# Performance work log

Hardware: AMD Instinct MI355X
Metric: run time of the kernel (lower is better)

Reference implementation:

```python
import jax, jax.numpy as jnp
import numpy as np

B, S, D, H, W = 8, 2048, 128, 8, 64
INT_HEADS = 8          # hardcoded in SpatioTemporalLayer1
EPS_COS = 1e-8
EPS_LN = 1e-5


def _mha(q_in, k_in, v_in, in_w, in_b, out_w, out_b, nh, mask=None):
    # q_in/k_in/v_in: (batch, len, d); torch nn.MultiheadAttention math (eval, no dropout)
    b, lq, d = q_in.shape
    hd = d // nh
    q = (q_in @ in_w[:d].T + in_b[:d]).reshape(b, lq, nh, hd)
    k = (k_in @ in_w[d:2 * d].T + in_b[d:2 * d]).reshape(b, k_in.shape[1], nh, hd)
    v = (v_in @ in_w[2 * d:].T + in_b[2 * d:]).reshape(b, v_in.shape[1], nh, hd)
    scores = jnp.einsum('bihd,bjhd->bhij', q, k) / jnp.sqrt(jnp.asarray(hd, q_in.dtype))
    if mask is not None:
        scores = scores + mask
    attn = jax.nn.softmax(scores, axis=-1)
    out = jnp.einsum('bhij,bjhd->bihd', attn, v).reshape(b, lq, d)
    return out @ out_w.T + out_b


def _layernorm(x, g, b):
    mu = x.mean(-1, keepdims=True)
    var = ((x - mu) ** 2).mean(-1, keepdims=True)
    return (x - mu) * jax.lax.rsqrt(var + EPS_LN) * g + b


def _cos_normalize(e):
    n = jnp.maximum(jnp.linalg.norm(e, axis=-1, keepdims=True), EPS_COS)
    return e / n


def _forward(x, spatial_info, temporal_info,
             lw_in_w, lw_in_b, lw_out_w, lw_out_b,
             spat_w, spat_b, temp_w, temp_b,
             int_in_w, int_in_b, int_out_w, int_out_b,
             ffn_w1, ffn_b1, ffn_w2, ffn_b2,
             ln1_g, ln1_b, ln2_g, ln2_b):
    b, s, d = x.shape
    # --- local window attention (S % W == 0 here, so no padding path) ---
    nw = s // W
    xw = x.reshape(b * nw, W, d)
    causal = jnp.triu(jnp.full((W, W), -jnp.inf, x.dtype), k=1)
    attn = _mha(xw, xw, xw, lw_in_w, lw_in_b, lw_out_w, lw_out_b, H, causal).reshape(b, s, d)
    x = _layernorm(attn + x, ln1_g, ln1_b)
    # --- FFN (torch nn.GELU default = exact erf) ---
    h = jax.nn.gelu(x @ ffn_w1.T + ffn_b1, approximate=False)
    x = _layernorm(h @ ffn_w2.T + ffn_b2 + x, ln2_g, ln2_b)
    # --- spatio-temporal interaction ---
    se = spatial_info @ spat_w.T + spat_b
    te = temporal_info @ temp_w.T + temp_b
    sn = _cos_normalize(se)
    tn = _cos_normalize(te)
    ss = jnp.einsum('bid,bjd->bij', sn, sn)   # (B,S,S) spatial cosine sim
    ts = jnp.einsum('bid,bjd->bij', tn, tn)   # (B,S,S) temporal cosine sim
    # interaction MHA is batch_first=False: it treats (B,S,D) as (len=B, batch=S, d).
    # Equivalent batch-first call on swapped axes (faithful to the torch source).
    inter = jnp.swapaxes(
        _mha(jnp.swapaxes(se, 0, 1), jnp.swapaxes(te, 0, 1), jnp.swapaxes(te, 0, 1),
             int_in_w, int_in_b, int_out_w, int_out_b, INT_HEADS), 0, 1)
    # similarity[b,i,j,d] = ss[b,i,j]*ts[b,i,j]*inter[b,i,d]; mean over j factorizes:
    sim = (ss * ts).mean(axis=2)              # (B,S)
    return x + sim[..., None] * inter


def setup_inputs() -> dict:
    key = jax.random.key(0)
    ks = jax.random.split(key, 24)
    sc = 0.02
    inp = {
        'x': jax.random.normal(ks[0], (B, S, D), jnp.float32),
        'spatial_info': jax.random.normal(ks[1], (B, S, D), jnp.float32),
        'temporal_info': jax.random.normal(ks[2], (B, S, D), jnp.float32),
        'lw_in_w': jax.random.normal(ks[3], (3 * D, D), jnp.float32) * sc,
        'lw_in_b': jnp.zeros((3 * D,), jnp.float32),
        'lw_out_w': jax.random.normal(ks[4], (D, D), jnp.float32) * sc,
        'lw_out_b': jnp.zeros((D,), jnp.float32),
        'spat_w': jax.random.normal(ks[5], (D, D), jnp.float32) * sc,
        'spat_b': jnp.zeros((D,), jnp.float32),
        'temp_w': jax.random.normal(ks[6], (D, D), jnp.float32) * sc,
        'temp_b': jnp.zeros((D,), jnp.float32),
        'int_in_w': jax.random.normal(ks[7], (3 * D, D), jnp.float32) * sc,
        'int_in_b': jnp.zeros((3 * D,), jnp.float32),
        'int_out_w': jax.random.normal(ks[8], (D, D), jnp.float32) * sc,
        'int_out_b': jnp.zeros((D,), jnp.float32),
        'ffn_w1': jax.random.normal(ks[9], (4 * D, D), jnp.float32) * sc,
        'ffn_b1': jnp.zeros((4 * D,), jnp.float32),
        'ffn_w2': jax.random.normal(ks[10], (D, 4 * D), jnp.float32) * sc,
        'ffn_b2': jnp.zeros((D,), jnp.float32),
        'ln1_g': jnp.ones((D,), jnp.float32),
        'ln1_b': jnp.zeros((D,), jnp.float32),
        'ln2_g': jnp.ones((D,), jnp.float32),
        'ln2_b': jnp.zeros((D,), jnp.float32),
    }
    return inp


def reference(x, spatial_info, temporal_info,
              lw_in_w, lw_in_b, lw_out_w, lw_out_b,
              spat_w, spat_b, temp_w, temp_b,
              int_in_w, int_in_b, int_out_w, int_out_b,
              ffn_w1, ffn_b1, ffn_w2, ffn_b2,
              ln1_g, ln1_b, ln2_g, ln2_b):
    return _forward(x, spatial_info, temporal_info,
                    lw_in_w, lw_in_b, lw_out_w, lw_out_b,
                    spat_w, spat_b, temp_w, temp_b,
                    int_in_w, int_in_b, int_out_w, int_out_b,
                    ffn_w1, ffn_b1, ffn_w2, ffn_b2,
                    ln1_g, ln1_b, ln2_g, ln2_b)
```

## Files before the change

### kernel.cpp

```cpp
#include <hip/hip_runtime.h>
#include <math.h>

#define BB 8
#define SS 2048
#define NTOK (BB * SS)
#define ATB_SPLIT 16

using bf16x8 = __attribute__((ext_vector_type(8))) short;
using f32x4  = __attribute__((ext_vector_type(4))) float;

__device__ __forceinline__ float gelu_tanh(float x) {
    float y = 0.7978845608f * (x + 0.044715f * x * x * x);
    float e = __expf(2.0f * y);
    float t = 1.0f - 2.0f / (e + 1.0f);
    return 0.5f * x * (1.0f + t);
}
__device__ __forceinline__ unsigned short f2b(float f) {
    unsigned int u = __float_as_uint(f);
    u += 0x7FFFu + ((u >> 16) & 1u);
    return (unsigned short)(u >> 16);
}
__device__ __forceinline__ float b2f(unsigned short u) {
    return __uint_as_float((unsigned int)u << 16);
}
__device__ __forceinline__ bf16x8 ldg_f32_b8(const float* p) {
    float4 f0 = *(const float4*)p, f1 = *(const float4*)(p + 4);
    union { ushort4 u[2]; bf16x8 v; } r;
    r.u[0] = (ushort4){f2b(f0.x), f2b(f0.y), f2b(f0.z), f2b(f0.w)};
    r.u[1] = (ushort4){f2b(f1.x), f2b(f1.y), f2b(f1.z), f2b(f1.w)};
    return r.v;
}

__global__ __launch_bounds__(256) void phaseA(
    const float* __restrict__ x,
    const float* __restrict__ lw_in_w, const float* __restrict__ b_in,
    const float* __restrict__ lw_out_w, const float* __restrict__ b_out,
    const float* __restrict__ lng, const float* __restrict__ lnb,
    float* __restrict__ x1, unsigned short* __restrict__ x1b,
    const float* __restrict__ ffn_w1, const float* __restrict__ ffn_w2,
    unsigned short* __restrict__ Wb)
{
    __shared__ unsigned short Qs[64 * 136];
    __shared__ unsigned short Ks[64 * 136];
    __shared__ unsigned short Vt[128 * 72];
    __shared__ unsigned short Pb[4][32 * 72];
    __shared__ float red[2][64][2];
    const int tid = threadIdx.x;

    if (blockIdx.x >= 256) {
        int i = (blockIdx.x - 256) * 256 + tid;
        float v = (i < 65536) ? ffn_w1[i] : ffn_w2[i - 65536];
        Wb[i] = f2b(v);
        return;
    }

    const int m0 = blockIdx.x * 64;
    const int wv = tid >> 6, lane = tid & 63, ln = lane & 15, q = lane >> 4;
    const int wm = (wv >> 1) * 32, wn = (wv & 1) * 64;

    bf16x8 afr[4][2];
    #pragma unroll
    for (int kf = 0; kf < 4; ++kf)
        #pragma unroll
        for (int fm = 0; fm < 2; ++fm)
            afr[kf][fm] = ldg_f32_b8(x + (size_t)(m0 + wm + fm * 16 + ln) * 128 + kf * 32 + q * 8);

    #pragma unroll
    for (int p = 0; p < 3; ++p) {
        f32x4 acc[2][4] = {};
        #pragma unroll
        for (int kf = 0; kf < 4; ++kf) {
            bf16x8 b[4];
            #pragma unroll
            for (int fn = 0; fn < 4; ++fn)
                b[fn] = ldg_f32_b8(lw_in_w + (size_t)(p * 128 + wn + fn * 16 + ln) * 128 + kf * 32 + q * 8);
            #pragma unroll
            for (int fm = 0; fm < 2; ++fm)
                #pragma unroll
                for (int fn = 0; fn < 4; ++fn)
                    acc[fm][fn] = __builtin_amdgcn_mfma_f32_16x16x32_bf16(afr[kf][fm], b[fn], acc[fm][fn], 0, 0, 0);
        }
        #pragma unroll
        for (int fm = 0; fm < 2; ++fm)
            #pragma unroll
            for (int r = 0; r < 4; ++r) {
                int rl = wm + fm * 16 + q * 4 + r;
                #pragma unroll
                for (int fn = 0; fn < 4; ++fn) {
                    int col = wn + fn * 16 + ln;
                    unsigned short v = f2b(acc[fm][fn][r] + b_in[p * 128 + col]);
                    if (p == 0)      Qs[rl * 136 + col] = v;
                    else if (p == 1) Ks[rl * 136 + col] = v;
                    else             Vt[col * 72 + rl] = v;
                }
            }
    }
    __syncthreads();

    {
        const int mh = wv >> 1, hq = wv & 1;
        unsigned short* P = &Pb[wv][0];
        #pragma unroll
        for (int hh = 0; hh < 4; ++hh) {
            const int h = hq * 4 + hh;
            f32x4 sacc[2][4] = {};
            bf16x8 az[2] = {}, bz[4] = {};
            if (q < 2) {
                #pragma unroll
                for (int fm = 0; fm < 2; ++fm)
                    az[fm] = *(const bf16x8*)&Qs[(mh * 32 + fm * 16 + ln) * 136 + h * 16 + q * 8];
                #pragma unroll
                for (int fn = 0; fn < 4; ++fn)
                    bz[fn] = *(const bf16x8*)&Ks[(fn * 16 + ln) * 136 + h * 16 + q * 8];
            }
            #pragma unroll
            for (int fm = 0; fm < 2; ++fm)
                #pragma unroll
                for (int fn = 0; fn < 4; ++fn)
                    sacc[fm][fn] = __builtin_amdgcn_mfma_f32_16x16x32_bf16(az[fm], bz[fn], sacc[fm][fn], 0, 0, 0);
            float invr[2][4];
            #pragma unroll
            for (int fm = 0; fm < 2; ++fm)
                #pragma unroll
                for (int r = 0; r < 4; ++r) {
                    int gi = mh * 32 + fm * 16 + q * 4 + r;
                    float mx = -1e30f;
                    #pragma unroll
                    for (int fn = 0; fn < 4; ++fn) {
                        int j = fn * 16 + ln;
                        float s = sacc[fm][fn][r] * 0.25f;
                        if (j > gi) s = -1e30f;
                        sacc[fm][fn][r] = s;
                        mx = fmaxf(mx, s);
                    }
                    #pragma unroll
                    for (int off = 1; off < 16; off <<= 1)
                        mx = fmaxf(mx, __shfl_xor(mx, off, 64));
                    float sum = 0.0f;
                    #pragma unroll
                    for (int fn = 0; fn < 4; ++fn) {
                        float p_ = __expf(sacc[fm][fn][r] - mx);
                        sacc[fm][fn][r] = p_;
                        sum += p_;
                    }
                    #pragma unroll
                    for (int off = 1; off < 16; off <<= 1)
                        sum += __shfl_xor(sum, off, 64);
                    invr[fm][r] = 1.0f / sum;
                    #pragma unroll
                    for (int fn = 0; fn < 4; ++fn)
                        P[(fm * 16 + q * 4 + r) * 72 + fn * 16 + ln] = f2b(sacc[fm][fn][r]);
                }
            f32x4 oacc[2] = {};
            #pragma unroll
            for (int kf2 = 0; kf2 < 2; ++kf2) {
                bf16x8 pa[2], vb;
                #pragma unroll
                for (int fm = 0; fm < 2; ++fm)
                    pa[fm] = *(const bf16x8*)&P[(fm * 16 + ln) * 72 + kf2 * 32 + q * 8];
                vb = *(const bf16x8*)&Vt[(h * 16 + ln) * 72 + kf2 * 32 + q * 8];
                #pragma unroll
                for (int fm = 0; fm < 2; ++fm)
                    oacc[fm] = __builtin_amdgcn_mfma_f32_16x16x32_bf16(pa[fm], vb, oacc[fm], 0, 0, 0);
            }
            #pragma unroll
            for (int fm = 0; fm < 2; ++fm)
                #pragma unroll
                for (int r = 0; r < 4; ++r)
                    Qs[(mh * 32 + fm * 16 + q * 4 + r) * 136 + h * 16 + ln] =
                        f2b(oacc[fm][r] * invr[fm][r]);
        }
    }
    __syncthreads();

    f32x4 acc[2][4] = {};
    #pragma unroll
    for (int kf = 0; kf < 4; ++kf) {
        bf16x8 a[2], b[4];
        #pragma unroll
        for (int fm = 0; fm < 2; ++fm)
            a[fm] = *(const bf16x8*)&Qs[(wm + fm * 16 + ln) * 136 + kf * 32 + q * 8];
        #pragma unroll
        for (int fn = 0; fn < 4; ++fn)
            b[fn] = ldg_f32_b8(lw_out_w + (size_t)(wn + fn * 16 + ln) * 128 + kf * 32 + q * 8);
        #pragma unroll
        for (int fm = 0; fm < 2; ++fm)
            #pragma unroll
            for (int fn = 0; fn < 4; ++fn)
                acc[fm][fn] = __builtin_amdgcn_mfma_f32_16x16x32_bf16(a[fm], b[fn], acc[fm][fn], 0, 0, 0);
    }
    #pragma unroll
    for (int fm = 0; fm < 2; ++fm)
        #pragma unroll
        for (int r = 0; r < 4; ++r) {
            int rl = wm + fm * 16 + q * 4 + r;
            int row = m0 + rl;
            float s1 = 0.0f, s2 = 0.0f;
            #pragma unroll
            for (int fn = 0; fn < 4; ++fn) {
                int col = wn + fn * 16 + ln;
                float vv = acc[fm][fn][r] + b_out[col] + x[(size_t)row * 128 + col];
                acc[fm][fn][r] = vv;
                s1 += vv; s2 += vv * vv;
            }
            #pragma unroll
            for (int off = 1; off < 16; off <<= 1) {
                s1 += __shfl_xor(s1, off, 64);
                s2 += __shfl_xor(s2, off, 64);
            }
            if (ln == 0) { red[0][rl][wv & 1] = s1; red[1][rl][wv & 1] = s2; }
        }
    __syncthreads();
    #pragma unroll
    for (int fm = 0; fm < 2; ++fm)
        #pragma unroll
        for (int r = 0; r < 4; ++r) {
            int rl = wm + fm * 16 + q * 4 + r;
            int row = m0 + rl;
            float mu = (red[0][rl][0] + red[0][rl][1]) * (1.0f / 128.0f);
            float var = (red[1][rl][0] + red[1][rl][1]) * (1.0f / 128.0f) - mu * mu;
            float rs = rsqrtf(var + 1e-5f);
            #pragma unroll
            for (int fn = 0; fn < 4; ++fn) {
                int col = wn + fn * 16 + ln;
                float o = (acc[fm][fn][r] - mu) * rs * lng[col] + lnb[col];
                x1[(size_t)row * 128 + col] = o;
                x1b[(size_t)row * 128 + col] = f2b(o);
            }
        }
}

__global__ __launch_bounds__(256) void ffn_fused(
    const unsigned short* __restrict__ x1b, const float* __restrict__ x1,
    const unsigned short* __restrict__ w1, const unsigned short* __restrict__ w2,
    const float* __restrict__ b1, const float* __restrict__ b2,
    const float* __restrict__ lng, const float* __restrict__ lnb,
    float* __restrict__ x2)
{
    __shared__ unsigned short Xs[64 * 136];
    __shared__ unsigned short Hs[2][64 * 72];
    __shared__ float red[2][64][2];
    const int tid = threadIdx.x, t0 = blockIdx.x * 64;
    const int wv = tid >> 6, lane = tid & 63, ln = lane & 15, q = lane >> 4;
    const int wm = (wv >> 1) * 32;
    const int wn1 = (wv & 1) * 32, wn2 = (wv & 1) * 64;

    const uint4* X4 = (const uint4*)(x1b + (size_t)t0 * 128);
    #pragma unroll
    for (int t = 0; t < 4; ++t) {
        int idx = tid + t * 256;
        int r = idx >> 4, c = idx & 15;
        *(uint4*)&Xs[r * 136 + c * 8] = X4[r * 16 + c];
    }
    __syncthreads();

    bf16x8 xfr[4][2];
    #pragma unroll
    for (int kf = 0; kf < 4; ++kf)
        #pragma unroll
        for (int fm = 0; fm < 2; ++fm)
            xfr[kf][fm] = *(const bf16x8*)&Xs[(wm + fm * 16 + ln) * 136 + kf * 32 + q * 8];

    f32x4 acc2[2][4] = {};
    for (int ch = 0; ch < 8; ++ch) {
        const int hc0 = ch * 64;
        unsigned short* Hb = &Hs[ch & 1][0];
        f32x4 acc1[2][2] = {};
        #pragma unroll
        for (int kf = 0; kf < 4; ++kf) {
            bf16x8 b[2];
            #pragma unroll
            for (int fn = 0; fn < 2; ++fn)
                b[fn] = *(const bf16x8*)&w1[(size_t)(hc0 + wn1 + fn * 16 + ln) * 128 + kf * 32 + q * 8];
            #pragma unroll
            for (int fm = 0; fm < 2; ++fm)
                #pragma unroll
                for (int fn = 0; fn < 2; ++fn)
                    acc1[fm][fn] = __builtin_amdgcn_mfma_f32_16x16x32_bf16(xfr[kf][fm], b[fn], acc1[fm][fn], 0, 0, 0);
        }
        #pragma unroll
        for (int fm = 0; fm < 2; ++fm)
            #pragma unroll
            for (int fn = 0; fn < 2; ++fn)
                #pragma unroll
                for (int r = 0; r < 4; ++r) {
                    int rl = wm + fm * 16 + q * 4 + r;
                    int col = wn1 + fn * 16 + ln;
                    Hb[rl * 72 + col] = f2b(gelu_tanh(acc1[fm][fn][r] + b1[hc0 + col]));
                }
        __syncthreads();
        #pragma unroll
        for (int kf2 = 0; kf2 < 2; ++kf2) {
            bf16x8 a[2], b[4];
            #pragma unroll
            for (int fm = 0; fm < 2; ++fm)
                a[fm] = *(const bf16x8*)&Hb[(wm + fm * 16 + ln) * 72 + kf2 * 32 + q * 8];
            #pragma unroll
            for (int fn = 0; fn < 4; ++fn)
                b[fn] = *(const bf16x8*)&w2[(size_t)(wn2 + fn * 16 + ln) * 512 + hc0 + kf2 * 32 + q * 8];
            #pragma unroll
            for (int fm = 0; fm < 2; ++fm)
                #pragma unroll
                for (int fn = 0; fn < 4; ++fn)
                    acc2[fm][fn] = __builtin_amdgcn_mfma_f32_16x16x32_bf16(a[fm], b[fn], acc2[fm][fn], 0, 0, 0);
        }
    }
    #pragma unroll
    for (int fm = 0; fm < 2; ++fm)
        #pragma unroll
        for (int r = 0; r < 4; ++r) {
            int rl = wm + fm * 16 + q * 4 + r;
            int row = t0 + rl;
            float s1 = 0.0f, s2 = 0.0f;
            #pragma unroll
            for (int fn = 0; fn < 4; ++fn) {
                int col = wn2 + fn * 16 + ln;
                float vv = acc2[fm][fn][r] + b2[col] + x1[(size_t)row * 128 + col];
                acc2[fm][fn][r] = vv;
                s1 += vv; s2 += vv * vv;
            }
            #pragma unroll
            for (int off = 1; off < 16; off <<= 1) {
                s1 += __shfl_xor(s1, off, 64);
                s2 += __shfl_xor(s2, off, 64);
            }
            if (ln == 0) { red[0][rl][wv & 1] = s1; red[1][rl][wv & 1] = s2; }
        }
    __syncthreads();
    #pragma unroll
    for (int fm = 0; fm < 2; ++fm)
        #pragma unroll
        for (int r = 0; r < 4; ++r) {
            int rl = wm + fm * 16 + q * 4 + r;
            int row = t0 + rl;
            float mu = (red[0][rl][0] + red[0][rl][1]) * (1.0f / 128.0f);
            float var = (red[1][rl][0] + red[1][rl][1]) * (1.0f / 128.0f) - mu * mu;
            float rs = rsqrtf(var + 1e-5f);
            #pragma unroll
            for (int fn = 0; fn < 4; ++fn) {
                int col = wn2 + fn * 16 + ln;
                x2[(size_t)row * 128 + col] = (acc2[fm][fn][r] - mu) * rs * lng[col] + lnb[col];
            }
        }
}

__global__ __launch_bounds__(256) void stproj_kernel(
    const float* __restrict__ sp, const float* __restrict__ tp,
    const float* __restrict__ Wsp, const float* __restrict__ Wtp,
    const float* __restrict__ bsp, const float* __restrict__ btp,
    unsigned short* __restrict__ snb, unsigned short* __restrict__ tnb,
    unsigned short* __restrict__ seb, unsigned short* __restrict__ teb)
{
    __shared__ float red[64][2];
    const int tid = threadIdx.x, m0 = blockIdx.x * 64, y = blockIdx.y;
    const float* Af = y ? tp : sp;
    const float* Wf = y ? Wtp : Wsp;
    const float* bias = y ? btp : bsp;
    unsigned short* nb = y ? tnb : snb;
    unsigned short* raw = y ? teb : seb;
    const int wv = tid >> 6, lane = tid & 63, ln = lane & 15, q = lane >> 4;
    const int wm = (wv >> 1) * 32, wn = (wv & 1) * 64;

    f32x4 acc[2][4] = {};
    #pragma unroll
    for (int kf = 0; kf < 4; ++kf) {
        bf16x8 a[2], b[4];
        #pragma unroll
        for (int fm = 0; fm < 2; ++fm)
            a[fm] = ldg_f32_b8(Af + (size_t)(m0 + wm + fm * 16 + ln) * 128 + kf * 32 + q * 8);
        #pragma unroll
        for (int fn = 0; fn < 4; ++fn)
            b[fn] = ldg_f32_b8(Wf + (size_t)(wn + fn * 16 + ln) * 128 + kf * 32 + q * 8);
        #pragma unroll
        for (int fm = 0; fm < 2; ++fm)
            #pragma unroll
            for (int fn = 0; fn < 4; ++fn)
                acc[fm][fn] = __builtin_amdgcn_mfma_f32_16x16x32_bf16(a[fm], b[fn], acc[fm][fn], 0, 0, 0);
    }
    #pragma unroll
    for (int fm = 0; fm < 2; ++fm)
        #pragma unroll
        for (int r = 0; r < 4; ++r) {
            int rl = wm + fm * 16 + q * 4 + r;
            float s2 = 0.0f;
            #pragma unroll
            for (int fn = 0; fn < 4; ++fn) {
                int col = wn + fn * 16 + ln;
                float vv = acc[fm][fn][r] + bias[col];
                acc[fm][fn][r] = vv;
                s2 += vv * vv;
            }
            #pragma unroll
            for (int off = 1; off < 16; off <<= 1) s2 += __shfl_xor(s2, off, 64);
            if (ln == 0) red[rl][wv & 1] = s2;
        }
    __syncthreads();
    #pragma unroll
    for (int fm = 0; fm < 2; ++fm)
        #pragma unroll
        for (int r = 0; r < 4; ++r) {
            int rl = wm + fm * 16 + q * 4 + r;
            int row = m0 + rl;
            float inv = 1.0f / fmaxf(sqrtf(red[rl][0] + red[rl][1]), 1e-8f);
            #pragma unroll
            for (int fn = 0; fn < 4; ++fn) {
                int col = wn + fn * 16 + ln;
                float vv = acc[fm][fn][r];
                nb[(size_t)row * 128 + col] = f2b(vv * inv);
                raw[(size_t)row * 128 + col] = f2b(vv);
            }
        }
}

__global__ __launch_bounds__(256) void atb_split_kernel(
    const unsigned short* __restrict__ snb, const unsigned short* __restrict__ tnb,
    float* __restrict__ part)
{
    const int b = blockIdx.z / ATB_SPLIT;
    const int chunk = blockIdx.z % ATB_SPLIT;
    const int d0 = blockIdx.x * 64, e0 = blockIdx.y * 64;
    __shared__ float Ss[32][68];
    __shared__ float Ts[32][68];
    const int tid = threadIdx.x;
    const int tx = tid % 16, ty = tid / 16;
    const int jbase = chunk * (SS / ATB_SPLIT);
    float acc[4][4] = {};
    for (int j0 = jbase; j0 < jbase + SS / ATB_SPLIT; j0 += 32) {
        {
            int r = tid >> 3, c8 = (tid & 7) * 8;
            uint4 sv = *(const uint4*)&snb[(size_t)(b * SS + j0 + r) * 128 + d0 + c8];
            uint4 tv = *(const uint4*)&tnb[(size_t)(b * SS + j0 + r) * 128 + e0 + c8];
            const unsigned short* sp = (const unsigned short*)&sv;
            const unsigned short* tp = (const unsigned short*)&tv;
            #pragma unroll
            for (int c = 0; c < 8; ++c) {
                Ss[r][c8 + c] = b2f(sp[c]);
                Ts[r][c8 + c] = b2f(tp[c]);
            }
        }
        __syncthreads();
        #pragma unroll
        for (int kk = 0; kk < 32; ++kk) {
            float4 af = *(const float4*)&Ss[kk][ty * 4];
            float4 wf = *(const float4*)&Ts[kk][tx * 4];
            float a[4] = {af.x, af.y, af.z, af.w};
            float w[4] = {wf.x, wf.y, wf.z, wf.w};
            #pragma unroll
            for (int i = 0; i < 4; ++i)
                #pragma unroll
                for (int j = 0; j < 4; ++j)
                    acc[i][j] = fmaf(a[i], w[j], acc[i][j]);
        }
        __syncthreads();
    }
    float* pp = part + (size_t)(b * ATB_SPLIT + chunk) * 16384;
    #pragma unroll
    for (int i = 0; i < 4; ++i) {
        float4 ov = {acc[i][0], acc[i][1], acc[i][2], acc[i][3]};
        *(float4*)&pp[(size_t)(d0 + ty * 4 + i) * 128 + e0 + tx * 4] = ov;
    }
}

__global__ __launch_bounds__(256) void atb_reduce_kernel(
    const float* __restrict__ part, unsigned short* __restrict__ Mtb)
{
    int i = blockIdx.x * 256 + threadIdx.x;
    int b = i >> 14, rem = i & 16383;
    int e = rem >> 7, d = rem & 127;
    const float* pp = part + (size_t)b * ATB_SPLIT * 16384 + (size_t)d * 128 + e;
    float s = 0.0f;
    #pragma unroll
    for (int c = 0; c < ATB_SPLIT; ++c) s += pp[(size_t)c * 16384];
    Mtb[i] = f2b(s);
}

__global__ __launch_bounds__(256) void simgemm_kernel(
    const unsigned short* __restrict__ snb, const unsigned short* __restrict__ tnb,
    const unsigned short* __restrict__ Mtb, float* __restrict__ sim)
{
    __shared__ float red[64][2];
    const int tid = threadIdx.x, m0 = blockIdx.x * 64, b = m0 >> 11;
    const int wv = tid >> 6, lane = tid & 63, ln = lane & 15, q = lane >> 4;
    const int wm = (wv >> 1) * 32, wn = (wv & 1) * 64;

    f32x4 acc[2][4] = {};
    #pragma unroll
    for (int kf = 0; kf < 4; ++kf) {
        bf16x8 a[2], bb[4];
        #pragma unroll
        for (int fm = 0; fm < 2; ++fm)
            a[fm] = *(const bf16x8*)&snb[(size_t)(m0 + wm + fm * 16 + ln) * 128 + kf * 32 + q * 8];
        #pragma unroll
        for (int fn = 0; fn < 4; ++fn)
            bb[fn] = *(const bf16x8*)&Mtb[(size_t)b * 16384 + (size_t)(wn + fn * 16 + ln) * 128 + kf * 32 + q * 8];
        #pragma unroll
        for (int fm = 0; fm < 2; ++fm)
            #pragma unroll
            for (int fn = 0; fn < 4; ++fn)
                acc[fm][fn] = __builtin_amdgcn_mfma_f32_16x16x32_bf16(a[fm], bb[fn], acc[fm][fn], 0, 0, 0);
    }
    #pragma unroll
    for (int fm = 0; fm < 2; ++fm)
        #pragma unroll
        for (int r = 0; r < 4; ++r) {
            int rl = wm + fm * 16 + q * 4 + r;
            int row = m0 + rl;
            float s = 0.0f;
            #pragma unroll
            for (int fn = 0; fn < 4; ++fn) {
                int col = wn + fn * 16 + ln;
                s += acc[fm][fn][r] * b2f(tnb[(size_t)row * 128 + col]);
            }
            #pragma unroll
            for (int off = 1; off < 16; off <<= 1) s += __shfl_xor(s, off, 64);
            if (ln == 0) red[rl][wv & 1] = s;
        }
    __syncthreads();
    if (tid < 64) sim[m0 + tid] = (red[tid][0] + red[tid][1]) * (1.0f / (float)SS);
}

__global__ __launch_bounds__(256) void inter_block(
    const unsigned short* __restrict__ seb, const unsigned short* __restrict__ teb,
    const float* __restrict__ Wint,
    const float* __restrict__ b_int,
    const float* __restrict__ Wio,
    const float* __restrict__ b_io,
    const float* __restrict__ sim, const float* __restrict__ x2,
    float* __restrict__ out)
{
    __shared__ unsigned short Qs[64 * 136];
    __shared__ unsigned short KVs[64 * 256];
    const int tid = threadIdx.x, s0 = blockIdx.x * 8;
    const int wv = tid >> 6, lane = tid & 63, ln = lane & 15, q = lane >> 4;
    const int wm = (wv >> 1) * 32, wn = (wv & 1) * 64;

    bf16x8 afr[4][2];
    #pragma unroll
    for (int kf = 0; kf < 4; ++kf)
        #pragma unroll
        for (int fm = 0; fm < 2; ++fm) {
            int rl = wm + fm * 16 + ln;
            size_t g = (size_t)(rl >> 3) * 2048 + s0 + (rl & 7);
            afr[kf][fm] = *(const bf16x8*)&seb[g * 128 + kf * 32 + q * 8];
        }

    #pragma unroll
    for (int p = 0; p < 3; ++p) {
        if (p == 1) {
            #pragma unroll
            for (int kf = 0; kf < 4; ++kf)
                #pragma unroll
                for (int fm = 0; fm < 2; ++fm) {
                    int rl = wm + fm * 16 + ln;
                    size_t g = (size_t)(rl >> 3) * 2048 + s0 + (rl & 7);
                    afr[kf][fm] = *(const bf16x8*)&teb[g * 128 + kf * 32 + q * 8];
                }
        }
        f32x4 acc[2][4] = {};
        #pragma unroll
        for (int kf = 0; kf < 4; ++kf) {
            bf16x8 b[4];
            #pragma unroll
            for (int fn = 0; fn < 4; ++fn)
                b[fn] = ldg_f32_b8(Wint + (size_t)(p * 128 + wn + fn * 16 + ln) * 128 + kf * 32 + q * 8);
            #pragma unroll
            for (int fm = 0; fm < 2; ++fm)
                #pragma unroll
                for (int fn = 0; fn < 4; ++fn)
                    acc[fm][fn] = __builtin_amdgcn_mfma_f32_16x16x32_bf16(afr[kf][fm], b[fn], acc[fm][fn], 0, 0, 0);
        }
        #pragma unroll
        for (int fm = 0; fm < 2; ++fm)
            #pragma unroll
            for (int r = 0; r < 4; ++r) {
                int rl = wm + fm * 16 + q * 4 + r;
                #pragma unroll
                for (int fn = 0; fn < 4; ++fn) {
                    int col = wn + fn * 16 + ln;
                    unsigned short v = f2b(acc[fm][fn][r] + b_int[p * 128 + col]);
                    if (p == 0) Qs[rl * 136 + col] = v;
                    else        KVs[rl * 256 + (p - 1) * 128 + col] = v;
                }
            }
        __syncthreads();
    }

    #pragma unroll
    for (int tt = 0; tt < 2; ++tt) {
        int task = tid + tt * 256;
        int ss = task >> 6, h = (task >> 3) & 7, i = task & 7;
        int rq = i * 8 + ss;
        float qr[16];
        {
            uint4 q0 = *(const uint4*)&Qs[rq * 136 + h * 16];
            uint4 q1 = *(const uint4*)&Qs[rq * 136 + h * 16 + 8];
            const unsigned short* p0 = (const unsigned short*)&q0;
            const unsigned short* p1 = (const unsigned short*)&q1;
            #pragma unroll
            for (int c = 0; c < 8; ++c) { qr[c] = b2f(p0[c]); qr[8 + c] = b2f(p1[c]); }
        }
        float sc[8];
        #pragma unroll
        for (int j = 0; j < 8; ++j) {
            uint4 k0 = *(const uint4*)&KVs[(j * 8 + ss) * 256 + h * 16];
            uint4 k1 = *(const uint4*)&KVs[(j * 8 + ss) * 256 + h * 16 + 8];
            const unsigned short* kp0 = (const unsigned short*)&k0;
            const unsigned short* kp1 = (const unsigned short*)&k1;
            float s = 0.0f;
            #pragma unroll
            for (int c = 0; c < 8; ++c) {
                s = fmaf(qr[c], b2f(kp0[c]), s);
                s = fmaf(qr[8 + c], b2f(kp1[c]), s);
            }
            sc[j] = s * 0.25f;
        }
        float mx = -1e30f;
        #pragma unroll
        for (int j = 0; j < 8; ++j) mx = fmaxf(mx, sc[j]);
        float pe[8], se = 0.0f;
        #pragma unroll
        for (int j = 0; j < 8; ++j) { pe[j] = __expf(sc[j] - mx); se += pe[j]; }
        float inv = 1.0f / se;
        float o[16] = {};
        #pragma unroll
        for (int j = 0; j < 8; ++j) {
            uint4 v0 = *(const uint4*)&KVs[(j * 8 + ss) * 256 + 128 + h * 16];
            uint4 v1 = *(const uint4*)&KVs[(j * 8 + ss) * 256 + 128 + h * 16 + 8];
            const unsigned short* vp0 = (const unsigned short*)&v0;
            const unsigned short* vp1 = (const unsigned short*)&v1;
            #pragma unroll
            for (int c = 0; c < 8; ++c) {
                o[c]     += pe[j] * b2f(vp0[c]);
                o[8 + c] += pe[j] * b2f(vp1[c]);
            }
        }
        ushort4 w0 = (ushort4){f2b(o[0]*inv),  f2b(o[1]*inv),  f2b(o[2]*inv),  f2b(o[3]*inv)};
        ushort4 w1 = (ushort4){f2b(o[4]*inv),  f2b(o[5]*inv),  f2b(o[6]*inv),  f2b(o[7]*inv)};
        ushort4 w2 = (ushort4){f2b(o[8]*inv),  f2b(o[9]*inv),  f2b(o[10]*inv), f2b(o[11]*inv)};
        ushort4 w3 = (ushort4){f2b(o[12]*inv), f2b(o[13]*inv), f2b(o[14]*inv), f2b(o[15]*inv)};
        *(ushort4*)&Qs[rq * 136 + h * 16]      = w0;
        *(ushort4*)&Qs[rq * 136 + h * 16 + 4]  = w1;
        *(ushort4*)&Qs[rq * 136 + h * 16 + 8]  = w2;
        *(ushort4*)&Qs[rq * 136 + h * 16 + 12] = w3;
    }
    __syncthreads();

    f32x4 acc[2][4] = {};
    #pragma unroll
    for (int kf = 0; kf < 4; ++kf) {
        bf16x8 a[2], b[4];
        #pragma unroll
        for (int fm = 0; fm < 2; ++fm)
            a[fm] = *(const bf16x8*)&Qs[(wm + fm * 16 + ln) * 136 + kf * 32 + q * 8];
        #pragma unroll
        for (int fn = 0; fn < 4; ++fn)
            b[fn] = ldg_f32_b8(Wio + (size_t)(wn + fn * 16 + ln) * 128 + kf * 32 + q * 8);
        #pragma unroll
        for (int fm = 0; fm < 2; ++fm)
            #pragma unroll
            for (int fn = 0; fn < 4; ++fn)
                acc[fm][fn] = __builtin_amdgcn_mfma_f32_16x16x32_bf16(a[fm], b[fn], acc[fm][fn], 0, 0, 0);
    }
    #pragma unroll
    for (int fm = 0; fm < 2; ++fm)
        #pragma unroll
        for (int r = 0; r < 4; ++r) {
            int rl = wm + fm * 16 + q * 4 + r;
            size_t g = (size_t)(rl >> 3) * 2048 + s0 + (rl & 7);
            float sc = sim[g];
            #pragma unroll
            for (int fn = 0; fn < 4; ++fn) {
                int col = wn + fn * 16 + ln;
                out[g * 128 + col] = (acc[fm][fn][r] + b_io[col]) * sc + x2[g * 128 + col];
            }
        }
}

extern "C" void kernel_launch(void* const* d_in, const int* in_sizes, int n_in,
                              void* d_out, int out_size, void* d_ws, size_t ws_size,
                              hipStream_t stream)
{
    const float* x        = (const float*)d_in[0];
    const float* spatial  = (const float*)d_in[1];
    const float* temporal = (const float*)d_in[2];
    const float* lw_in_w  = (const float*)d_in[3];
    const float* lw_in_b  = (const float*)d_in[4];
    const float* lw_out_w = (const float*)d_in[5];
    const float* lw_out_b = (const float*)d_in[6];
    const float* spat_w   = (const float*)d_in[7];
    const float* spat_b   = (const float*)d_in[8];
    const float* temp_w   = (const float*)d_in[9];
    const float* temp_b   = (const float*)d_in[10];
    const float* int_in_w = (const float*)d_in[11];
    const float* int_in_b = (const float*)d_in[12];
    const float* int_out_w= (const float*)d_in[13];
    const float* int_out_b= (const float*)d_in[14];
    const float* ffn_w1   = (const float*)d_in[15];
    const float* ffn_b1   = (const float*)d_in[16];
    const float* ffn_w2   = (const float*)d_in[17];
    const float* ffn_b2   = (const float*)d_in[18];
    const float* ln1_g    = (const float*)d_in[19];
    const float* ln1_b    = (const float*)d_in[20];
    const float* ln2_g    = (const float*)d_in[21];
    const float* ln2_b    = (const float*)d_in[22];
    float* out = (float*)d_out;

    char* base = (char*)d_ws;
    float*          x1   = (float*)(base + 0);
    unsigned short* x1b  = (unsigned short*)(base + 8388608);
    float*          x2   = (float*)(base + 12582912);
    unsigned short* snb  = (unsigned short*)(base + 20971520);
    unsigned short* tnb  = (unsigned short*)(base + 25165824);
    unsigned short* seb  = (unsigned short*)(base + 29360128);
    unsigned short* teb  = (unsigned short*)(base + 33554432);
    unsigned short* Mtb  = (unsigned short*)(base + 37748736);
    float*          simb = (float*)(base + 38010880);
    unsigned short* Wb   = (unsigned short*)(base + 38076416);
    float*          part = x1;

    phaseA<<<768, 256, 0, stream>>>(
        x, lw_in_w, lw_in_b, lw_out_w, lw_out_b, ln1_g, ln1_b, x1, x1b,
        ffn_w1, ffn_w2, Wb);
    ffn_fused<<<256, 256, 0, stream>>>(
        x1b, x1, Wb, Wb + 65536, ffn_b1, ffn_b2, ln2_g, ln2_b, x2);
    stproj_kernel<<<dim3(256, 2), 256, 0, stream>>>(
        spatial, temporal, spat_w, temp_w, spat_b, temp_b,
        snb, tnb, seb, teb);
    atb_split_kernel<<<dim3(2, 2, 8 * ATB_SPLIT), 256, 0, stream>>>(snb, tnb, part);
    atb_reduce_kernel<<<512, 256, 0, stream>>>(part, Mtb);
    simgemm_kernel<<<256, 256, 0, stream>>>(snb, tnb, Mtb, simb);
    inter_block<<<2048 / 8, 256, 0, stream>>>(
        seb, teb, int_in_w, int_in_b, int_out_w, int_out_b, simb, x2, out);
}
```

Before: 249.3 us.

## Merge independent kernels into two heterogeneous launches to cut launch count

Folds the spatial/temporal projection and normalization into the first kernel as extra blocks alongside windowed attention and weight conversion. Folds the split A^T B partial reduction into the FFN kernel as extra blocks, using a shared memory pool. The partials buffer moves to its own workspace region because it can no longer alias x1 while the FFN reads it. This removes two launches and lets independent work overlap across CUs, at the cost of higher shared-memory footprint for the smaller block types and a larger workspace.

```diff
diff --git a/kernel.cpp b/kernel.cpp
--- a/kernel.cpp
+++ b/kernel.cpp
@@ -31,14 +31,19 @@
     return r.v;
 }
 
-__global__ __launch_bounds__(256) void phaseA(
+__global__ __launch_bounds__(256) void phase1(
     const float* __restrict__ x,
     const float* __restrict__ lw_in_w, const float* __restrict__ b_in,
     const float* __restrict__ lw_out_w, const float* __restrict__ b_out,
     const float* __restrict__ lng, const float* __restrict__ lnb,
     float* __restrict__ x1, unsigned short* __restrict__ x1b,
     const float* __restrict__ ffn_w1, const float* __restrict__ ffn_w2,
-    unsigned short* __restrict__ Wb)
+    unsigned short* __restrict__ Wb,
+    const float* __restrict__ spatial, const float* __restrict__ temporal,
+    const float* __restrict__ spat_w, const float* __restrict__ temp_w,
+    const float* __restrict__ bsp, const float* __restrict__ btp,
+    unsigned short* __restrict__ snb, unsigned short* __restrict__ tnb,
+    unsigned short* __restrict__ seb, unsigned short* __restrict__ teb)
 {
     __shared__ unsigned short Qs[64 * 136];
     __shared__ unsigned short Ks[64 * 136];
@@ -46,6 +51,70 @@
     __shared__ unsigned short Pb[4][32 * 72];
     __shared__ float red[2][64][2];
     const int tid = threadIdx.x;
+    const int wv = tid >> 6, lane = tid & 63, ln = lane & 15, q = lane >> 4;
+
+    if (blockIdx.x >= 768) {
+        const int idx2 = blockIdx.x - 768;
+        const int y = idx2 >> 8;
+        const int m0 = (idx2 & 255) * 64;
+        const float* Af = y ? temporal : spatial;
+        const float* Wf = y ? temp_w : spat_w;
+        const float* bias = y ? btp : bsp;
+        unsigned short* nb = y ? tnb : snb;
+        unsigned short* raw = y ? teb : seb;
+        const int wm = (wv >> 1) * 32, wn = (wv & 1) * 64;
+
+        f32x4 acc[2][4] = {};
+        #pragma unroll
+        for (int kf = 0; kf < 4; ++kf) {
+            bf16x8 a[2], b[4];
+            #pragma unroll
+            for (int fm = 0; fm < 2; ++fm)
+                a[fm] = ldg_f32_b8(Af + (size_t)(m0 + wm + fm * 16 + ln) * 128 + kf * 32 + q * 8);
+            #pragma unroll
+            for (int fn = 0; fn < 4; ++fn)
+                b[fn] = ldg_f32_b8(Wf + (size_t)(wn + fn * 16 + ln) * 128 + kf * 32 + q * 8);
+            #pragma unroll
+            for (int fm = 0; fm < 2; ++fm)
+                #pragma unroll
+                for (int fn = 0; fn < 4; ++fn)
+                    acc[fm][fn] = __builtin_amdgcn_mfma_f32_16x16x32_bf16(a[fm], b[fn], acc[fm][fn], 0, 0, 0);
+        }
+        #pragma unroll
+        for (int fm = 0; fm < 2; ++fm)
+            #pragma unroll
+            for (int r = 0; r < 4; ++r) {
+                int rl = wm + fm * 16 + q * 4 + r;
+                float s2 = 0.0f;
+                #pragma unroll
+                for (int fn = 0; fn < 4; ++fn) {
+                    int col = wn + fn * 16 + ln;
+                    float vv = acc[fm][fn][r] + bias[col];
+                    acc[fm][fn][r] = vv;
+                    s2 += vv * vv;
+                }
+                #pragma unroll
+                for (int off = 1; off < 16; off <<= 1) s2 += __shfl_xor(s2, off, 64);
+                if (ln == 0) red[0][rl][wv & 1] = s2;
+            }
+        __syncthreads();
+        #pragma unroll
+        for (int fm = 0; fm < 2; ++fm)
+            #pragma unroll
+            for (int r = 0; r < 4; ++r) {
+                int rl = wm + fm * 16 + q * 4 + r;
+                int row = m0 + rl;
+                float inv = 1.0f / fmaxf(sqrtf(red[0][rl][0] + red[0][rl][1]), 1e-8f);
+                #pragma unroll
+                for (int fn = 0; fn < 4; ++fn) {
+                    int col = wn + fn * 16 + ln;
+                    float vv = acc[fm][fn][r];
+                    nb[(size_t)row * 128 + col] = f2b(vv * inv);
+                    raw[(size_t)row * 128 + col] = f2b(vv);
+                }
+            }
+        return;
+    }
 
     if (blockIdx.x >= 256) {
         int i = (blockIdx.x - 256) * 256 + tid;
@@ -55,7 +124,6 @@
     }
 
     const int m0 = blockIdx.x * 64;
-    const int wv = tid >> 6, lane = tid & 63, ln = lane & 15, q = lane >> 4;
     const int wm = (wv >> 1) * 32, wn = (wv & 1) * 64;
 
     bf16x8 afr[4][2];
@@ -230,234 +298,174 @@
         }
 }
 
-__global__ __launch_bounds__(256) void ffn_fused(
+__global__ __launch_bounds__(256) void phase2(
     const unsigned short* __restrict__ x1b, const float* __restrict__ x1,
-    const unsigned short* __restrict__ w1, const unsigned short* __restrict__ w2,
+    const unsigned short* __restrict__ Wb,
     const float* __restrict__ b1, const float* __restrict__ b2,
     const float* __restrict__ lng, const float* __restrict__ lnb,
-    float* __restrict__ x2)
-{
-    __shared__ unsigned short Xs[64 * 136];
-    __shared__ unsigned short Hs[2][64 * 72];
-    __shared__ float red[2][64][2];
-    const int tid = threadIdx.x, t0 = blockIdx.x * 64;
-    const int wv = tid >> 6, lane = tid & 63, ln = lane & 15, q = lane >> 4;
-    const int wm = (wv >> 1) * 32;
-    const int wn1 = (wv & 1) * 32, wn2 = (wv & 1) * 64;
-
-    const uint4* X4 = (const uint4*)(x1b + (size_t)t0 * 128);
-    #pragma unroll
-    for (int t = 0; t < 4; ++t) {
-        int idx = tid + t * 256;
-        int r = idx >> 4, c = idx & 15;
-        *(uint4*)&Xs[r * 136 + c * 8] = X4[r * 16 + c];
-    }
-    __syncthreads();
-
-    bf16x8 xfr[4][2];
-    #pragma unroll
-    for (int kf = 0; kf < 4; ++kf)
-        #pragma unroll
-        for (int fm = 0; fm < 2; ++fm)
-            xfr[kf][fm] = *(const bf16x8*)&Xs[(wm + fm * 16 + ln) * 136 + kf * 32 + q * 8];
-
-    f32x4 acc2[2][4] = {};
-    for (int ch = 0; ch < 8; ++ch) {
-        const int hc0 = ch * 64;
-        unsigned short* Hb = &Hs[ch & 1][0];
-        f32x4 acc1[2][2] = {};
-        #pragma unroll
-        for (int kf = 0; kf < 4; ++kf) {
-            bf16x8 b[2];
-            #pragma unroll
-            for (int fn = 0; fn < 2; ++fn)
-                b[fn] = *(const bf16x8*)&w1[(size_t)(hc0 + wn1 + fn * 16 + ln) * 128 + kf * 32 + q * 8];
-            #pragma unroll
-            for (int fm = 0; fm < 2; ++fm)
-                #pragma unroll
-                for (int fn = 0; fn < 2; ++fn)
-                    acc1[fm][fn] = __builtin_amdgcn_mfma_f32_16x16x32_bf16(xfr[kf][fm], b[fn], acc1[fm][fn], 0, 0, 0);
-        }
-        #pragma unroll
-        for (int fm = 0; fm < 2; ++fm)
-            #pragma unroll
-            for (int fn = 0; fn < 2; ++fn)
-                #pragma unroll
-                for (int r = 0; r < 4; ++r) {
-                    int rl = wm + fm * 16 + q * 4 + r;
-                    int col = wn1 + fn * 16 + ln;
-                    Hb[rl * 72 + col] = f2b(gelu_tanh(acc1[fm][fn][r] + b1[hc0 + col]));
-                }
-        __syncthreads();
-        #pragma unroll
-        for (int kf2 = 0; kf2 < 2; ++kf2) {
-            bf16x8 a[2], b[4];
-            #pragma unroll
-            for (int fm = 0; fm < 2; ++fm)
-                a[fm] = *(const bf16x8*)&Hb[(wm + fm * 16 + ln) * 72 + kf2 * 32 + q * 8];
-            #pragma unroll
-            for (int fn = 0; fn < 4; ++fn)
-                b[fn] = *(const bf16x8*)&w2[(size_t)(wn2 + fn * 16 + ln) * 512 + hc0 + kf2 * 32 + q * 8];
-            #pragma unroll
-            for (int fm = 0; fm < 2; ++fm)
-                #pragma unroll
-                for (int fn = 0; fn < 4; ++fn)
-                    acc2[fm][fn] = __builtin_amdgcn_mfma_f32_16x16x32_bf16(a[fm], b[fn], acc2[fm][fn], 0, 0, 0);
-        }
-    }
-    #pragma unroll
-    for (int fm = 0; fm < 2; ++fm)
-        #pragma unroll
-        for (int r = 0; r < 4; ++r) {
-            int rl = wm + fm * 16 + q * 4 + r;
-            int row = t0 + rl;
-            float s1 = 0.0f, s2 = 0.0f;
-            #pragma unroll
-            for (int fn = 0; fn < 4; ++fn) {
-                int col = wn2 + fn * 16 + ln;
-                float vv = acc2[fm][fn][r] + b2[col] + x1[(size_t)row * 128 + col];
-                acc2[fm][fn][r] = vv;
-                s1 += vv; s2 += vv * vv;
-            }
-            #pragma unroll
-            for (int off = 1; off < 16; off <<= 1) {
-                s1 += __shfl_xor(s1, off, 64);
-                s2 += __shfl_xor(s2, off, 64);
-            }
-            if (ln == 0) { red[0][rl][wv & 1] = s1; red[1][rl][wv & 1] = s2; }
-        }
-    __syncthreads();
-    #pragma unroll
-    for (int fm = 0; fm < 2; ++fm)
-        #pragma unroll
-        for (int r = 0; r < 4; ++r) {
-            int rl = wm + fm * 16 + q * 4 + r;
-            int row = t0 + rl;
-            float mu = (red[0][rl][0] + red[0][rl][1]) * (1.0f / 128.0f);
-            float var = (red[1][rl][0] + red[1][rl][1]) * (1.0f / 128.0f) - mu * mu;
-            float rs = rsqrtf(var + 1e-5f);
-            #pragma unroll
-            for (int fn = 0; fn < 4; ++fn) {
-                int col = wn2 + fn * 16 + ln;
-                x2[(size_t)row * 128 + col] = (acc2[fm][fn][r] - mu) * rs * lng[col] + lnb[col];
-            }
-        }
-}
-
-__global__ __launch_bounds__(256) void stproj_kernel(
-    const float* __restrict__ sp, const float* __restrict__ tp,
-    const float* __restrict__ Wsp, const float* __restrict__ Wtp,
-    const float* __restrict__ bsp, const float* __restrict__ btp,
-    unsigned short* __restrict__ snb, unsigned short* __restrict__ tnb,
-    unsigned short* __restrict__ seb, unsigned short* __restrict__ teb)
-{
-    __shared__ float red[64][2];
-    const int tid = threadIdx.x, m0 = blockIdx.x * 64, y = blockIdx.y;
-    const float* Af = y ? tp : sp;
-    const float* Wf = y ? Wtp : Wsp;
-    const float* bias = y ? btp : bsp;
-    unsigned short* nb = y ? tnb : snb;
-    unsigned short* raw = y ? teb : seb;
-    const int wv = tid >> 6, lane = tid & 63, ln = lane & 15, q = lane >> 4;
-    const int wm = (wv >> 1) * 32, wn = (wv & 1) * 64;
-
-    f32x4 acc[2][4] = {};
-    #pragma unroll
-    for (int kf = 0; kf < 4; ++kf) {
-        bf16x8 a[2], b[4];
-        #pragma unroll
-        for (int fm = 0; fm < 2; ++fm)
-            a[fm] = ldg_f32_b8(Af + (size_t)(m0 + wm + fm * 16 + ln) * 128 + kf * 32 + q * 8);
-        #pragma unroll
-        for (int fn = 0; fn < 4; ++fn)
-            b[fn] = ldg_f32_b8(Wf + (size_t)(wn + fn * 16 + ln) * 128 + kf * 32 + q * 8);
-        #pragma unroll
-        for (int fm = 0; fm < 2; ++fm)
-            #pragma unroll
-            for (int fn = 0; fn < 4; ++fn)
-                acc[fm][fn] = __builtin_amdgcn_mfma_f32_16x16x32_bf16(a[fm], b[fn], acc[fm][fn], 0, 0, 0);
-    }
-    #pragma unroll
-    for (int fm = 0; fm < 2; ++fm)
-        #pragma unroll
-        for (int r = 0; r < 4; ++r) {
-            int rl = wm + fm * 16 + q * 4 + r;
-            float s2 = 0.0f;
-            #pragma unroll
-            for (int fn = 0; fn < 4; ++fn) {
-                int col = wn + fn * 16 + ln;
-                float vv = acc[fm][fn][r] + bias[col];
-                acc[fm][fn][r] = vv;
-                s2 += vv * vv;
-            }
-            #pragma unroll
-            for (int off = 1; off < 16; off <<= 1) s2 += __shfl_xor(s2, off, 64);
-            if (ln == 0) red[rl][wv & 1] = s2;
-        }
-    __syncthreads();
-    #pragma unroll
-    for (int fm = 0; fm < 2; ++fm)
-        #pragma unroll
-        for (int r = 0; r < 4; ++r) {
-            int rl = wm + fm * 16 + q * 4 + r;
-            int row = m0 + rl;
-            float inv = 1.0f / fmaxf(sqrtf(red[rl][0] + red[rl][1]), 1e-8f);
-            #pragma unroll
-            for (int fn = 0; fn < 4; ++fn) {
-                int col = wn + fn * 16 + ln;
-                float vv = acc[fm][fn][r];
-                nb[(size_t)row * 128 + col] = f2b(vv * inv);
-                raw[(size_t)row * 128 + col] = f2b(vv);
-            }
-        }
-}
-
-__global__ __launch_bounds__(256) void atb_split_kernel(
+    float* __restrict__ x2,
     const unsigned short* __restrict__ snb, const unsigned short* __restrict__ tnb,
     float* __restrict__ part)
 {
-    const int b = blockIdx.z / ATB_SPLIT;
-    const int chunk = blockIdx.z % ATB_SPLIT;
-    const int d0 = blockIdx.x * 64, e0 = blockIdx.y * 64;
-    __shared__ float Ss[32][68];
-    __shared__ float Ts[32][68];
+    __shared__ __align__(16) char pool[36864];
+    __shared__ float red[2][64][2];
     const int tid = threadIdx.x;
-    const int tx = tid % 16, ty = tid / 16;
-    const int jbase = chunk * (SS / ATB_SPLIT);
-    float acc[4][4] = {};
-    for (int j0 = jbase; j0 < jbase + SS / ATB_SPLIT; j0 += 32) {
-        {
-            int r = tid >> 3, c8 = (tid & 7) * 8;
-            uint4 sv = *(const uint4*)&snb[(size_t)(b * SS + j0 + r) * 128 + d0 + c8];
-            uint4 tv = *(const uint4*)&tnb[(size_t)(b * SS + j0 + r) * 128 + e0 + c8];
-            const unsigned short* sp = (const unsigned short*)&sv;
-            const unsigned short* tp = (const unsigned short*)&tv;
-            #pragma unroll
-            for (int c = 0; c < 8; ++c) {
-                Ss[r][c8 + c] = b2f(sp[c]);
-                Ts[r][c8 + c] = b2f(tp[c]);
-            }
+    const int wv = tid >> 6, lane = tid & 63, ln = lane & 15, q = lane >> 4;
+
+    if (blockIdx.x < 256) {
+        unsigned short* Xs = (unsigned short*)pool;
+        unsigned short* Hs0 = (unsigned short*)(pool + 17408);
+        unsigned short* Hs1 = (unsigned short*)(pool + 26624);
+        const int t0 = blockIdx.x * 64;
+        const int wm = (wv >> 1) * 32;
+        const int wn1 = (wv & 1) * 32, wn2 = (wv & 1) * 64;
+        const unsigned short* w1 = Wb;
+        const unsigned short* w2 = Wb + 65536;
+
+        const uint4* X4 = (const uint4*)(x1b + (size_t)t0 * 128);
+        #pragma unroll
+        for (int t = 0; t < 4; ++t) {
+            int idx = tid + t * 256;
+            int r = idx >> 4, c = idx & 15;
+            *(uint4*)&Xs[r * 136 + c * 8] = X4[r * 16 + c];
         }
         __syncthreads();
-        #pragma unroll
-        for (int kk = 0; kk < 32; ++kk) {
-            float4 af = *(const float4*)&Ss[kk][ty * 4];
-            float4 wf = *(const float4*)&Ts[kk][tx * 4];
-            float a[4] = {af.x, af.y, af.z, af.w};
-            float w[4] = {wf.x, wf.y, wf.z, wf.w};
-            #pragma unroll
-            for (int i = 0; i < 4; ++i)
-                #pragma unroll
-                for (int j = 0; j < 4; ++j)
-                    acc[i][j] = fmaf(a[i], w[j], acc[i][j]);
-        }
+
+        bf16x8 xfr[4][2];
+        #pragma unroll
+        for (int kf = 0; kf < 4; ++kf)
+            #pragma unroll
+            for (int fm = 0; fm < 2; ++fm)
+                xfr[kf][fm] = *(const bf16x8*)&Xs[(wm + fm * 16 + ln) * 136 + kf * 32 + q * 8];
+
+        f32x4 acc2[2][4] = {};
+        for (int ch = 0; ch < 8; ++ch) {
+            const int hc0 = ch * 64;
+            unsigned short* Hb = (ch & 1) ? Hs1 : Hs0;
+            f32x4 acc1[2][2] = {};
+            #pragma unroll
+            for (int kf = 0; kf < 4; ++kf) {
+                bf16x8 b[2];
+                #pragma unroll
+                for (int fn = 0; fn < 2; ++fn)
+                    b[fn] = *(const bf16x8*)&w1[(size_t)(hc0 + wn1 + fn * 16 + ln) * 128 + kf * 32 + q * 8];
+                #pragma unroll
+                for (int fm = 0; fm < 2; ++fm)
+                    #pragma unroll
+                    for (int fn = 0; fn < 2; ++fn)
+                        acc1[fm][fn] = __builtin_amdgcn_mfma_f32_16x16x32_bf16(xfr[kf][fm], b[fn], acc1[fm][fn], 0, 0, 0);
+            }
+            #pragma unroll
+            for (int fm = 0; fm < 2; ++fm)
+                #pragma unroll
+                for (int fn = 0; fn < 2; ++fn)
+                    #pragma unroll
+                    for (int r = 0; r < 4; ++r) {
+                        int rl = wm + fm * 16 + q * 4 + r;
+                        int col = wn1 + fn * 16 + ln;
+                        Hb[rl * 72 + col] = f2b(gelu_tanh(acc1[fm][fn][r] + b1[hc0 + col]));
+                    }
+            __syncthreads();
+            #pragma unroll
+            for (int kf2 = 0; kf2 < 2; ++kf2) {
+                bf16x8 a[2], b[4];
+                #pragma unroll
+                for (int fm = 0; fm < 2; ++fm)
+                    a[fm] = *(const bf16x8*)&Hb[(wm + fm * 16 + ln) * 72 + kf2 * 32 + q * 8];
+                #pragma unroll
+                for (int fn = 0; fn < 4; ++fn)
+                    b[fn] = *(const bf16x8*)&w2[(size_t)(wn2 + fn * 16 + ln) * 512 + hc0 + kf2 * 32 + q * 8];
+                #pragma unroll
+                for (int fm = 0; fm < 2; ++fm)
+                    #pragma unroll
+                    for (int fn = 0; fn < 4; ++fn)
+                        acc2[fm][fn] = __builtin_amdgcn_mfma_f32_16x16x32_bf16(a[fm], b[fn], acc2[fm][fn], 0, 0, 0);
+            }
+        }
+        #pragma unroll
+        for (int fm = 0; fm < 2; ++fm)
+            #pragma unroll
+            for (int r = 0; r < 4; ++r) {
+                int rl = wm + fm * 16 + q * 4 + r;
+                int row = t0 + rl;
+                float s1 = 0.0f, s2 = 0.0f;
+                #pragma unroll
+                for (int fn = 0; fn < 4; ++fn) {
+                    int col = wn2 + fn * 16 + ln;
+                    float vv = acc2[fm][fn][r] + b2[col] + x1[(size_t)row * 128 + col];
+                    acc2[fm][fn][r] = vv;
+                    s1 += vv; s2 += vv * vv;
+                }
+                #pragma unroll
+                for (int off = 1; off < 16; off <<= 1) {
+                    s1 += __shfl_xor(s1, off, 64);
+                    s2 += __shfl_xor(s2, off, 64);
+                }
+                if (ln == 0) { red[0][rl][wv & 1] = s1; red[1][rl][wv & 1] = s2; }
+            }
         __syncthreads();
-    }
-    float* pp = part + (size_t)(b * ATB_SPLIT + chunk) * 16384;
-    #pragma unroll
-    for (int i = 0; i < 4; ++i) {
-        float4 ov = {acc[i][0], acc[i][1], acc[i][2], acc[i][3]};
-        *(float4*)&pp[(size_t)(d0 + ty * 4 + i) * 128 + e0 + tx * 4] = ov;
+        #pragma unroll
+        for (int fm = 0; fm < 2; ++fm)
+            #pragma unroll
+            for (int r = 0; r < 4; ++r) {
+                int rl = wm + fm * 16 + q * 4 + r;
+                int row = t0 + rl;
+                float mu = (red[0][rl][0] + red[0][rl][1]) * (1.0f / 128.0f);
+                float var = (red[1][rl][0] + red[1][rl][1]) * (1.0f / 128.0f) - mu * mu;
+                float rs = rsqrtf(var + 1e-5f);
+                #pragma unroll
+                for (int fn = 0; fn < 4; ++fn) {
+                    int col = wn2 + fn * 16 + ln;
+                    x2[(size_t)row * 128 + col] = (acc2[fm][fn][r] - mu) * rs * lng[col] + lnb[col];
+                }
+            }
+        return;
+    }
+
+    {
+        float* Ss = (float*)pool;
+        float* Ts = (float*)(pool + 8704);
+        const int idx2 = blockIdx.x - 256;
+        const int d0 = (idx2 & 1) * 64, e0 = ((idx2 >> 1) & 1) * 64;
+        const int z = idx2 >> 2;
+        const int b = z >> 4, chunk = z & 15;
+        const int tx = tid % 16, ty = tid / 16;
+        const int jbase = chunk * (SS / ATB_SPLIT);
+        float acc[4][4] = {};
+        for (int j0 = jbase; j0 < jbase + SS / ATB_SPLIT; j0 += 32) {
+            {
+                int r = tid >> 3, c8 = (tid & 7) * 8;
+                uint4 sv = *(const uint4*)&snb[(size_t)(b * SS + j0 + r) * 128 + d0 + c8];
+                uint4 tv = *(const uint4*)&tnb[(size_t)(b * SS + j0 + r) * 128 + e0 + c8];
+                const unsigned short* sp = (const unsigned short*)&sv;
+                const unsigned short* tp = (const unsigned short*)&tv;
+                #pragma unroll
+                for (int c = 0; c < 8; ++c) {
+                    Ss[r * 68 + c8 + c] = b2f(sp[c]);
+                    Ts[r * 68 + c8 + c] = b2f(tp[c]);
+                }
+            }
+            __syncthreads();
+            #pragma unroll
+            for (int kk = 0; kk < 32; ++kk) {
+                float4 af = *(const float4*)&Ss[kk * 68 + ty * 4];
+                float4 wf = *(const float4*)&Ts[kk * 68 + tx * 4];
+                float a[4] = {af.x, af.y, af.z, af.w};
+                float w[4] = {wf.x, wf.y, wf.z, wf.w};
+                #pragma unroll
+                for (int i = 0; i < 4; ++i)
+                    #pragma unroll
+                    for (int j = 0; j < 4; ++j)
+                        acc[i][j] = fmaf(a[i], w[j], acc[i][j]);
+            }
+            __syncthreads();
+        }
+        float* pp = part + (size_t)(b * ATB_SPLIT + chunk) * 16384;
+        #pragma unroll
+        for (int i = 0; i < 4; ++i) {
+            float4 ov = {acc[i][0], acc[i][1], acc[i][2], acc[i][3]};
+            *(float4*)&pp[(size_t)(d0 + ty * 4 + i) * 128 + e0 + tx * 4] = ov;
+        }
     }
 }
 
@@ -695,9 +703,7 @@
     const float* int_in_b = (const float*)d_in[12];
     const float* int_out_w= (const float*)d_in[13];
     const float* int_out_b= (const float*)d_in[14];
-    const float* ffn_w1   = (const float*)d_in[15];
     const float* ffn_b1   = (const float*)d_in[16];
-    const float* ffn_w2   = (const float*)d_in[17];
     const float* ffn_b2   = (const float*)d_in[18];
     const float* ln1_g    = (const float*)d_in[19];
     const float* ln1_b    = (const float*)d_in[20];
@@ -716,19 +722,17 @@
     unsigned short* Mtb  = (unsigned short*)(base + 37748736);
     float*          simb = (float*)(base + 38010880);
     unsigned short* Wb   = (unsigned short*)(base + 38076416);
-    float*          part = x1;
-
-    phaseA<<<768, 256, 0, stream>>>(
+    float*          part = (float*)(base + 38338560);
+
+    phase1<<<1280, 256, 0, stream>>>(
         x, lw_in_w, lw_in_b, lw_out_w, lw_out_b, ln1_g, ln1_b, x1, x1b,
-        ffn_w1, ffn_w2, Wb);
-    ffn_fused<<<256, 256, 0, stream>>>(
-        x1b, x1, Wb, Wb + 65536, ffn_b1, ffn_b2, ln2_g, ln2_b, x2);
-    stproj_kernel<<<dim3(256, 2), 256, 0, stream>>>(
+        (const float*)d_in[15], (const float*)d_in[17], Wb,
         spatial, temporal, spat_w, temp_w, spat_b, temp_b,
         snb, tnb, seb, teb);
-    atb_split_kernel<<<dim3(2, 2, 8 * ATB_SPLIT), 256, 0, stream>>>(snb, tnb, part);
+    phase2<<<768, 256, 0, stream>>>(
+        x1b, x1, Wb, ffn_b1, ffn_b2, ln2_g, ln2_b, x2, snb, tnb, part);
     atb_reduce_kernel<<<512, 256, 0, stream>>>(part, Mtb);
     simgemm_kernel<<<256, 256, 0, stream>>>(snb, tnb, Mtb, simb);
-    inter_block<<<2048 / 8, 256, 0, stream>>>(
+    inter_block<<<256, 256, 0, stream>>>(
         seb, teb, int_in_w, int_in_b, int_out_w, int_out_b, simb, x2, out);
 }
```

Measured after the change: 242.1 us. -2.9%, faster.
